# Performance work log

Measured on AMD Instinct MI355X. Metric: run time of the kernel, lower is better.

## Reference

```python
import jax, jax.numpy as jnp
import numpy as np

N_ATOMS = 16384
N_EDGES = 65536
ATOM_DIM = 29
BOND_DIM = 8
UNITS = 64          # message_units / embed_dim
STEPS = 4
HEADS = 8
DENSE = 512
B_MOL = 256         # molecules
T_ATOMS = 64        # atoms per molecule (N_ATOMS = B_MOL * T_ATOMS)


def setup_inputs() -> dict:
    key = jax.random.key(0)
    ks = jax.random.split(key, 24)
    D = UNITS

    atom_features = jax.random.normal(ks[0], (N_ATOMS, ATOM_DIM), jnp.float32)
    bond_features = jax.random.normal(ks[1], (N_EDGES, BOND_DIM), jnp.float32)
    # edges within molecules
    mol = jax.random.randint(ks[2], (N_EDGES,), 0, B_MOL)
    a = jax.random.randint(ks[3], (N_EDGES,), 0, T_ATOMS)
    b = jax.random.randint(ks[4], (N_EDGES,), 0, T_ATOMS)
    pair_indices = jnp.stack([mol * T_ATOMS + a, mol * T_ATOMS + b], axis=1).astype(jnp.int32)
    molecule_indicator = (jnp.arange(N_ATOMS) // T_ATOMS).astype(jnp.int32)

    def xavier(k, shape, fan_in):
        return jax.random.normal(k, shape, jnp.float32) * (1.0 / np.sqrt(fan_in))

    params = dict(
        kernel=xavier(ks[5], (BOND_DIM, D * D), BOND_DIM),
        kernel_bias=jnp.zeros((D * D,), jnp.float32),
        gru_w_ih=xavier(ks[6], (3 * D, D), D),
        gru_w_hh=xavier(ks[7], (3 * D, D), D),
        gru_b_ih=jnp.zeros((3 * D,), jnp.float32),
        gru_b_hh=jnp.zeros((3 * D,), jnp.float32),
        in_proj_w=xavier(ks[8], (3 * D, D), D),
        in_proj_b=jnp.zeros((3 * D,), jnp.float32),
        out_proj_w=xavier(ks[9], (D, D), D),
        out_proj_b=jnp.zeros((D,), jnp.float32),
        ffn_w1=xavier(ks[10], (D, DENSE), D),
        ffn_b1=jnp.zeros((DENSE,), jnp.float32),
        ffn_w2=xavier(ks[11], (DENSE, D), DENSE),
        ffn_b2=jnp.zeros((D,), jnp.float32),
        ln1_g=jnp.ones((D,), jnp.float32),
        ln1_b=jnp.zeros((D,), jnp.float32),
        ln2_g=jnp.ones((D,), jnp.float32),
        ln2_b=jnp.zeros((D,), jnp.float32),
        d1_w=xavier(ks[12], (D, DENSE), D),
        d1_b=jnp.zeros((DENSE,), jnp.float32),
        d2_w=xavier(ks[13], (DENSE, 1), DENSE),
        d2_b=jnp.zeros((1,), jnp.float32),
    )
    return dict(atom_features=atom_features, bond_features=bond_features,
                pair_indices=pair_indices, molecule_indicator=molecule_indicator, **params)


def _layernorm(x, g, b, eps=1e-5):
    mu = x.mean(-1, keepdims=True)
    var = ((x - mu) ** 2).mean(-1, keepdims=True)
    return (x - mu) * jax.lax.rsqrt(var + eps) * g + b


def _forward(atom_features, bond_features, pair_indices, molecule_indicator,
             kernel, kernel_bias, gru_w_ih, gru_w_hh, gru_b_ih, gru_b_hh,
             in_proj_w, in_proj_b, out_proj_w, out_proj_b,
             ffn_w1, ffn_b1, ffn_w2, ffn_b2, ln1_g, ln1_b, ln2_g, ln2_b,
             d1_w, d1_b, d2_w, d2_b):
    D = UNITS
    n = atom_features.shape[0]
    # pad atom features to message_units
    h = jnp.pad(atom_features, ((0, 0), (0, D - atom_features.shape[1])))

    src = pair_indices[:, 0]
    dst = pair_indices[:, 1]
    # per-edge bond-conditioned transform matrices: [E, D, D]
    bond_mat = (bond_features @ kernel + kernel_bias).reshape(-1, D, D)

    for _ in range(STEPS):
        nbr = h[dst]                                      # gather [E, D]
        msg = jnp.einsum('eij,ej->ei', bond_mat, nbr)     # per-edge matvec
        agg = jax.ops.segment_sum(msg, src, num_segments=n)  # scatter-add [N, D]
        # GRUCell(input=agg, hidden=h)
        gi = agg @ gru_w_ih.T + gru_b_ih
        gh = h @ gru_w_hh.T + gru_b_hh
        i_r, i_z, i_n = jnp.split(gi, 3, axis=-1)
        h_r, h_z, h_n = jnp.split(gh, 3, axis=-1)
        r = jax.nn.sigmoid(i_r + h_r)
        z = jax.nn.sigmoid(i_z + h_z)
        nn_ = jnp.tanh(i_n + r * h_n)
        h = (1.0 - z) * nn_ + z * h

    # PartitionPadding: scatter atoms into [B_MOL, T_ATOMS, D] (indicator sorted, contiguous)
    starts = jnp.searchsorted(molecule_indicator, jnp.arange(B_MOL, dtype=molecule_indicator.dtype))
    pos = jnp.arange(n) - starts[molecule_indicator]
    x = jnp.zeros((B_MOL, T_ATOMS, D), h.dtype).at[molecule_indicator, pos].set(h)

    valid = jnp.any(x != 0, axis=-1)                      # [B, T] key-padding mask

    # multi-head self-attention
    qkv = x @ in_proj_w.T + in_proj_b                     # [B, T, 3D]
    q, k, v = jnp.split(qkv, 3, axis=-1)
    hd = D // HEADS
    q = q.reshape(B_MOL, T_ATOMS, HEADS, hd)
    k = k.reshape(B_MOL, T_ATOMS, HEADS, hd)
    v = v.reshape(B_MOL, T_ATOMS, HEADS, hd)
    scores = jnp.einsum('bqhd,bkhd->bhqk', q, k) / np.sqrt(hd)
    scores = jnp.where(valid[:, None, None, :], scores, -1e9)
    attn = jax.nn.softmax(scores, axis=-1)
    ao = jnp.einsum('bhqk,bkhd->bqhd', attn, v).reshape(B_MOL, T_ATOMS, D)
    ao = ao @ out_proj_w.T + out_proj_b

    y1 = _layernorm(x + ao, ln1_g, ln1_b)
    ffn = jax.nn.relu(y1 @ ffn_w1 + ffn_b1) @ ffn_w2 + ffn_b2
    y2 = _layernorm(y1 + ffn, ln2_g, ln2_b)
    pooled = y2.mean(axis=1)                              # [B, D]

    out = jax.nn.relu(pooled @ d1_w + d1_b)
    return jax.nn.sigmoid(out @ d2_w + d2_b)              # [B, 1]


def reference(atom_features, bond_features, pair_indices, molecule_indicator,
              kernel, kernel_bias, gru_w_ih, gru_w_hh, gru_b_ih, gru_b_hh,
              in_proj_w, in_proj_b, out_proj_w, out_proj_b,
              ffn_w1, ffn_b1, ffn_w2, ffn_b2, ln1_g, ln1_b, ln2_g, ln2_b,
              d1_w, d1_b, d2_w, d2_b):
    return _forward(atom_features, bond_features, pair_indices, molecule_indicator,
                    kernel, kernel_bias, gru_w_ih, gru_w_hh, gru_b_ih, gru_b_hh,
                    in_proj_w, in_proj_b, out_proj_w, out_proj_b,
                    ffn_w1, ffn_b1, ffn_w2, ffn_b2, ln1_g, ln1_b, ln2_g, ln2_b,
                    d1_w, d1_b, d2_w, d2_b)
```

## Files before the change

kernel.cpp:

```cpp
#include <hip/hip_runtime.h>
#include <hip/hip_bf16.h>
#include <math.h>

#define NA 16384
#define NE 65536
#define AD 29

typedef __attribute__((ext_vector_type(8))) short bfrag8;
typedef __attribute__((ext_vector_type(4))) float f32x4;

__device__ __forceinline__ float sigmoidf_(float x) { return 1.0f / (1.0f + expf(-x)); }
__device__ __forceinline__ unsigned short bf16bits(float x) {
  __hip_bfloat16 hb = __float2bfloat16(x);
  return *reinterpret_cast<unsigned short*>(&hb);
}
__device__ __forceinline__ float bf16val(unsigned short u) {
  unsigned int b = ((unsigned int)u) << 16;
  return __uint_as_float(b);
}

__global__ void k_init_h(const float* __restrict__ af, float* __restrict__ h,
                         int* __restrict__ count) {
  int idx = blockIdx.x * 256 + threadIdx.x;
  if (idx >= NA * 64) return;
  if (idx < NA) count[idx] = 0;
  int a = idx >> 6, d = idx & 63;
  h[idx] = (d < AD) ? af[a * AD + d] : 0.0f;
}

__global__ void k_prep_KrA(const float* __restrict__ kern, const float* __restrict__ kbias,
                           unsigned short* __restrict__ KrA) {
  int idx = blockIdx.x * 256 + threadIdx.x;
  if (idx >= 36864) return;
  int r = idx & 7;
  int tmp = idx >> 3;
  int lane = tmp & 63;
  int tmp2 = tmp >> 6;
  int ks = tmp2 % 18, w = tmp2 / 18;
  int i = w * 16 + (lane & 15);
  int kj = ks * 32 + ((lane >> 4) << 3) + r;
  int k9 = kj >> 6, j = kj & 63;
  float v = (k9 < 8) ? kern[k9 * 4096 + i * 64 + j] : kbias[i * 64 + j];
  KrA[idx] = bf16bits(v);
}

__global__ void k_prep_Wg(const float* __restrict__ wih, const float* __restrict__ whh,
                          unsigned short* __restrict__ Wh, unsigned short* __restrict__ Wl) {
  int idx = blockIdx.x * 256 + threadIdx.x;
  if (idx >= 24576) return;
  int r = idx & 7;
  int lane = (idx >> 3) & 63;
  int t2 = idx >> 9;
  int ks = t2 & 1;
  int t3 = t2 >> 1;
  int q = t3 % 6, w = t3 / 6;
  int s = q / 3, g = q % 3;
  int R = g * 64 + w * 16 + (lane & 15);
  int kk = ks * 32 + ((lane >> 4) << 3) + r;
  float v = (s == 0) ? wih[R * 64 + kk] : whh[R * 64 + kk];
  unsigned short hi = bf16bits(v);
  Wh[idx] = hi;
  Wl[idx] = bf16bits(v - bf16val(hi));
}

__global__ void k_prep_Wffn(const float* __restrict__ w1, const float* __restrict__ w2,
                            unsigned short* __restrict__ W1h, unsigned short* __restrict__ W1l,
                            unsigned short* __restrict__ W2h, unsigned short* __restrict__ W2l) {
  int idx = blockIdx.x * 256 + threadIdx.x;
  if (idx >= 65536) return;
  int r = idx & 7;
  int lane = (idx >> 3) & 63;
  int rest = (idx >> 9) & 63;
  if (idx < 32768) {
    int tile = rest >> 1, ks = rest & 1;
    int hid = tile * 16 + (lane & 15);
    int kk = ks * 32 + ((lane >> 4) << 3) + r;
    float v = w1[kk * 512 + hid];
    unsigned short hi = bf16bits(v);
    W1h[idx] = hi;
    W1l[idx] = bf16bits(v - bf16val(hi));
  } else {
    int i2 = idx - 32768;
    int tile = rest >> 4, ks = rest & 15;
    int out = tile * 16 + (lane & 15);
    int kk = ks * 32 + ((lane >> 4) << 3) + r;
    float v = w2[kk * 64 + out];
    unsigned short hi = bf16bits(v);
    W2h[i2] = hi;
    W2l[i2] = bf16bits(v - bf16val(hi));
  }
}

__global__ void k_count(const int* __restrict__ pairs, int* __restrict__ count) {
  int e = blockIdx.x * 256 + threadIdx.x;
  if (e >= NE) return;
  atomicAdd(&count[pairs[2 * e]], 1);
}
__global__ void k_scan1(const int* __restrict__ count, int* __restrict__ bsum) {
  __shared__ int red[256];
  int b = blockIdx.x, t = threadIdx.x;
  red[t] = count[b * 256 + t];
  __syncthreads();
  for (int s = 128; s > 0; s >>= 1) { if (t < s) red[t] += red[t + s]; __syncthreads(); }
  if (t == 0) bsum[b] = red[0];
}
__global__ void k_scan2(const int* __restrict__ count, const int* __restrict__ bsum,
                        int* __restrict__ start, int* __restrict__ cursor) {
  __shared__ int sc[256];
  __shared__ int basev;
  int b = blockIdx.x, t = threadIdx.x;
  if (t == 0) { int s = 0; for (int i = 0; i < b; ++i) s += bsum[i]; basev = s; }
  int v = count[b * 256 + t];
  sc[t] = v;
  __syncthreads();
  for (int off = 1; off < 256; off <<= 1) {
    int add = (t >= off) ? sc[t - off] : 0;
    __syncthreads();
    sc[t] += add;
    __syncthreads();
  }
  int excl = sc[t] - v + basev;
  start[b * 256 + t] = excl;
  cursor[b * 256 + t] = excl;
  if (b * 256 + t == NA - 1) start[NA] = excl + v;
}
__global__ void k_place(const int* __restrict__ pairs, int* __restrict__ cursor,
                        int* __restrict__ elist) {
  int e = blockIdx.x * 256 + threadIdx.x;
  if (e >= NE) return;
  int pos = atomicAdd(&cursor[pairs[2 * e]], 1);
  elist[pos] = e;
}
__global__ void k_reorder(const float* __restrict__ bf, const int* __restrict__ pairs,
                          const int* __restrict__ elist, int* __restrict__ sdst,
                          float* __restrict__ sbf) {
  int idx = blockIdx.x * 256 + threadIdx.x;
  if (idx >= NE * 8) return;
  int pos = idx >> 3, k = idx & 7;
  int e = elist[pos];
  sbf[idx] = bf[e * 8 + k];
  if (k == 0) sdst[pos] = pairs[2 * e + 1];
}

#define MW 4
#define MAW 4
__global__ __launch_bounds__(256, 4) void k_msg(
    const float* __restrict__ h_in, const int* __restrict__ start,
    const int* __restrict__ sdst, const float* __restrict__ sbf,
    const unsigned short* __restrict__ KrA,
    const unsigned short* __restrict__ Wh, const unsigned short* __restrict__ Wl,
    const float* __restrict__ bih, const float* __restrict__ bhh,
    float* __restrict__ h_out) {
  __shared__ __align__(16) unsigned short Tb[16 * 584];
  __shared__ __align__(16) unsigned short Xh[16 * 136];
  __shared__ __align__(16) unsigned short Xl[16 * 136];
  __shared__ __align__(16) float Hf[16 * 68];
  __shared__ __align__(16) float AHa[16 * 68];
  __shared__ float bias_s[384];
  const int tid = threadIdx.x, lane = tid & 63, wv = tid >> 6;
  const int ablk = blockIdx.x * 16;
  const int awave = ablk + wv * MAW;

#pragma unroll
  for (int aa = 0; aa < MAW; ++aa) {
    const int a = wv * MAW + aa;
    const float v = h_in[(ablk + a) * 64 + lane];
    Hf[a * 68 + lane] = v;
    const unsigned short hi = bf16bits(v);
    Xh[a * 136 + 64 + lane] = hi;
    Xl[a * 136 + 64 + lane] = bf16bits(v - bf16val(hi));
  }
  if (tid < 192) { bias_s[tid] = bih[tid]; bias_s[192 + tid] = bhh[tid]; }

  for (int a = 0; a < MAW; ++a) {
    const int s0 = __builtin_amdgcn_readfirstlane(start[awave + a]);
    const int s1 = __builtin_amdgcn_readfirstlane(start[awave + a + 1]);
    float t[9] = {0.f, 0.f, 0.f, 0.f, 0.f, 0.f, 0.f, 0.f, 0.f};
    for (int base = s0; base < s1; base += 8) {
      const int nb = s1 - base;
      float hv[8];
#pragma unroll
      for (int i = 0; i < 8; ++i) {
        int d = (i < nb) ? sdst[base + i] : 0;
        hv[i] = (i < nb) ? h_in[d * 64 + lane] : 0.f;
      }
#pragma unroll
      for (int i = 0; i < 8; ++i) {
#pragma unroll
        for (int k = 0; k < 8; ++k)
          t[k] = fmaf(sbf[(base + i) * 8 + k], hv[i], t[k]);
        t[8] += hv[i];
      }
    }
    const int row = wv * MAW + a;
#pragma unroll
    for (int k = 0; k < 9; ++k) Tb[row * 584 + k * 64 + lane] = bf16bits(t[k]);
  }
  __syncthreads();

  f32x4 acc = {0.f, 0.f, 0.f, 0.f};
  const bfrag8* KrA8 = reinterpret_cast<const bfrag8*>(KrA);
  const int tb_base = (lane & 15) * 584 + ((lane >> 4) << 3);
#pragma unroll 3
  for (int ks = 0; ks < 18; ++ks) {
    bfrag8 af = KrA8[(wv * 18 + ks) * 64 + lane];
    bfrag8 bfr = *reinterpret_cast<const bfrag8*>(&Tb[tb_base + ks * 32]);
    acc = __builtin_amdgcn_mfma_f32_16x16x32_bf16(af, bfr, acc, 0, 0, 0);
  }
#pragma unroll
  for (int reg = 0; reg < 4; ++reg) {
    const int ii = wv * 16 + ((lane >> 4) << 2) + reg;
    const unsigned short hi = bf16bits(acc[reg]);
    Xh[(lane & 15) * 136 + ii] = hi;
    Xl[(lane & 15) * 136 + ii] = bf16bits(acc[reg] - bf16val(hi));
  }
  __syncthreads();

  const bfrag8* Wh8 = reinterpret_cast<const bfrag8*>(Wh);
  const bfrag8* Wl8 = reinterpret_cast<const bfrag8*>(Wl);
  f32x4 g0 = {0,0,0,0}, g1 = {0,0,0,0}, g2 = {0,0,0,0};
  f32x4 g3 = {0,0,0,0}, g4 = {0,0,0,0}, g5 = {0,0,0,0};
  f32x4* gptr[6] = {&g0, &g1, &g2, &g3, &g4, &g5};
#pragma unroll
  for (int q = 0; q < 6; ++q) {
    const int s = q / 3;
    f32x4 g = *gptr[q];
#pragma unroll
    for (int ks = 0; ks < 2; ++ks) {
      const int fidx = ((wv * 6 + q) * 2 + ks) * 64 + lane;
      bfrag8 Ah = Wh8[fidx];
      bfrag8 Al = Wl8[fidx];
      const int xoff = (lane & 15) * 136 + (s * 2 + ks) * 32 + ((lane >> 4) << 3);
      bfrag8 Bh = *reinterpret_cast<const bfrag8*>(&Xh[xoff]);
      bfrag8 Bl = *reinterpret_cast<const bfrag8*>(&Xl[xoff]);
      g = __builtin_amdgcn_mfma_f32_16x16x32_bf16(Ah, Bh, g, 0, 0, 0);
      g = __builtin_amdgcn_mfma_f32_16x16x32_bf16(Ah, Bl, g, 0, 0, 0);
      g = __builtin_amdgcn_mfma_f32_16x16x32_bf16(Al, Bh, g, 0, 0, 0);
    }
    *gptr[q] = g;
  }
#pragma unroll
  for (int reg = 0; reg < 4; ++reg) {
    const int i = wv * 16 + ((lane >> 4) << 2) + reg;
    const int atom = lane & 15;
    const float r = sigmoidf_(g0[reg] + bias_s[i] + g3[reg] + bias_s[192 + i]);
    const float z = sigmoidf_(g1[reg] + bias_s[64 + i] + g4[reg] + bias_s[256 + i]);
    const float nn = tanhf(g2[reg] + bias_s[128 + i] + r * (g5[reg] + bias_s[320 + i]));
    const float hold = Hf[atom * 68 + i];
    AHa[atom * 68 + i] = (1.0f - z) * nn + z * hold;
  }
  __syncthreads();
#pragma unroll
  for (int aa = 0; aa < MAW; ++aa) {
    const int a = wv * MAW + aa;
    h_out[(ablk + a) * 64 + lane] = AHa[a * 68 + lane];
  }
}

#define QABLK 4
__global__ __launch_bounds__(256, 2) void k_qkv(
    const float* __restrict__ h, const float* __restrict__ w,
    const float* __restrict__ b, float* __restrict__ qkv,
    int* __restrict__ valid) {
  __shared__ __align__(16) float w_s[192 * 64];
  __shared__ __align__(16) float x_s[4][QABLK][64];
  const int tid = threadIdx.x, lane = tid & 63, wv = tid >> 6;
  for (int idx = tid; idx < 192 * 64; idx += 256) {
    int r = idx >> 6, d = idx & 63;
    w_s[(r << 6) + ((((d >> 2) ^ (r & 7)) << 2) | (d & 3))] = w[idx];
  }
  __syncthreads();
  const float4* w4 = reinterpret_cast<const float4*>(w_s);
  const float bq = b[lane], bk = b[64 + lane], bv_ = b[128 + lane];
  const int swz = lane & 7;
  const int gw = blockIdx.x * 4 + wv;
  const int stride = gridDim.x * 4 * QABLK;
  for (int ag = gw * QABLK; ag < NA; ag += stride) {
#pragma unroll
    for (int e = 0; e < QABLK; ++e) x_s[wv][e][lane] = h[(ag + e) * 64 + lane];
    __syncthreads();
    const float4* x4 = reinterpret_cast<const float4*>(&x_s[wv][0][0]);
    float aq[QABLK] = {0,0,0,0}, ak[QABLK] = {0,0,0,0}, av_[QABLK] = {0,0,0,0};
    int nz[QABLK] = {0,0,0,0};
#pragma unroll 4
    for (int d4 = 0; d4 < 16; ++d4) {
      int sl = d4 ^ swz;
      float4 wq = w4[(lane << 4) + sl];
      float4 wk = w4[((lane + 64) << 4) + sl];
      float4 wvv = w4[((lane + 128) << 4) + sl];
#pragma unroll
      for (int e = 0; e < QABLK; ++e) {
        float4 xv = x4[e * 16 + d4];
        aq[e] += wq.x*xv.x + wq.y*xv.y + wq.z*xv.z + wq.w*xv.w;
        ak[e] += wk.x*xv.x + wk.y*xv.y + wk.z*xv.z + wk.w*xv.w;
        av_[e] += wvv.x*xv.x + wvv.y*xv.y + wvv.z*xv.z + wvv.w*xv.w;
        nz[e] |= (int)(xv.x != 0.f) | (int)(xv.y != 0.f) | (int)(xv.z != 0.f) | (int)(xv.w != 0.f);
      }
    }
#pragma unroll
    for (int e = 0; e < QABLK; ++e) {
      qkv[(ag + e) * 192 + lane] = aq[e] + bq;
      qkv[(ag + e) * 192 + 64 + lane] = ak[e] + bk;
      qkv[(ag + e) * 192 + 128 + lane] = av_[e] + bv_;
      if (lane == 0) valid[ag + e] = nz[e];
    }
    __syncthreads();
  }
}

__global__ void k_attn(const float* __restrict__ qkv, const int* __restrict__ valid,
                       float* __restrict__ ao) {
  const int b = blockIdx.x >> 3, hh = blockIdx.x & 7;
  __shared__ float k_s[64][8];
  __shared__ float v_s[64][8];
  __shared__ int vd_s[64];
  const int lane = threadIdx.x;
  const int rowbase = (b * 64 + lane) * 192;
#pragma unroll
  for (int j = 0; j < 8; ++j) {
    k_s[lane][j] = qkv[rowbase + 64 + hh * 8 + j];
    v_s[lane][j] = qkv[rowbase + 128 + hh * 8 + j];
  }
  vd_s[lane] = valid[b * 64 + lane];
  __syncthreads();
  float q[8];
#pragma unroll
  for (int j = 0; j < 8; ++j) q[j] = qkv[rowbase + hh * 8 + j];
  float m = -3.0e38f, l = 0.f, o[8] = {0,0,0,0,0,0,0,0};
  for (int t = 0; t < 64; ++t) {
    float s = 0.f;
#pragma unroll
    for (int j = 0; j < 8; ++j) s += q[j] * k_s[t][j];
    s *= 0.35355339059327373f;
    s = vd_s[t] ? s : -1.0e9f;
    float mn = fmaxf(m, s);
    float c = expf(m - mn);
    float p = expf(s - mn);
    l = l * c + p;
#pragma unroll
    for (int j = 0; j < 8; ++j) o[j] = o[j] * c + p * v_s[t][j];
    m = mn;
  }
  const float inv = 1.0f / l;
  const int obase = (b * 64 + lane) * 64 + hh * 8;
#pragma unroll
  for (int j = 0; j < 8; ++j) ao[obase + j] = o[j] * inv;
}

#define OABLK 4
__global__ __launch_bounds__(256, 1) void k_out_ln1(
    const float* __restrict__ x, const float* __restrict__ ao,
    const float* __restrict__ w, const float* __restrict__ bias,
    const float* __restrict__ g, const float* __restrict__ bb,
    float* __restrict__ y1) {
  __shared__ __align__(16) float w_s[64 * 64];
  __shared__ __align__(16) float a_s[4][OABLK][64];
  const int tid = threadIdx.x, lane = tid & 63, wv = tid >> 6;
  for (int idx = tid; idx < 64 * 64; idx += 256) {
    int r = idx >> 6, d = idx & 63;
    w_s[(r << 6) + ((((d >> 2) ^ (r & 7)) << 2) | (d & 3))] = w[idx];
  }
  __syncthreads();
  const float4* w4 = reinterpret_cast<const float4*>(w_s);
  const float bo = bias[lane], gg = g[lane], bbb = bb[lane];
  const int swz = lane & 7;
  const int gw = blockIdx.x * 4 + wv;
  const int stride = gridDim.x * 4 * OABLK;
  for (int ag = gw * OABLK; ag < NA; ag += stride) {
#pragma unroll
    for (int e = 0; e < OABLK; ++e) a_s[wv][e][lane] = ao[(ag + e) * 64 + lane];
    __syncthreads();
    const float4* a4 = reinterpret_cast<const float4*>(&a_s[wv][0][0]);
    float acc[OABLK] = {0,0,0,0};
#pragma unroll 4
    for (int d4 = 0; d4 < 16; ++d4) {
      int sl = d4 ^ swz;
      float4 wr = w4[(lane << 4) + sl];
#pragma unroll
      for (int e = 0; e < OABLK; ++e) {
        float4 av = a4[e * 16 + d4];
        acc[e] += wr.x*av.x + wr.y*av.y + wr.z*av.z + wr.w*av.w;
      }
    }
#pragma unroll
    for (int e = 0; e < OABLK; ++e) {
      float val = acc[e] + bo + x[(ag + e) * 64 + lane];
      float s1 = val, s2 = val * val;
#pragma unroll
      for (int mm = 1; mm < 64; mm <<= 1) {
        s1 += __shfl_xor(s1, mm, 64);
        s2 += __shfl_xor(s2, mm, 64);
      }
      float mu = s1 * 0.015625f;
      float var = s2 * 0.015625f - mu * mu;
      y1[(ag + e) * 64 + lane] = (val - mu) * rsqrtf(var + 1e-5f) * gg + bbb;
    }
    __syncthreads();
  }
}

__global__ __launch_bounds__(256, 3) void k_ffn(
    const float* __restrict__ y1,
    const unsigned short* __restrict__ W1h, const unsigned short* __restrict__ W1l,
    const unsigned short* __restrict__ W2h, const unsigned short* __restrict__ W2l,
    const float* __restrict__ b1, const float* __restrict__ b2,
    const float* __restrict__ g, const float* __restrict__ bb,
    float* __restrict__ y2) {
  __shared__ __align__(16) unsigned short Xh[16 * 72];
  __shared__ __align__(16) unsigned short Xl[16 * 72];
  __shared__ __align__(16) unsigned short Hh[16 * 520];
  __shared__ __align__(16) unsigned short Hl[16 * 520];
  __shared__ __align__(16) float Y1f[16 * 68];
  __shared__ __align__(16) float Of[16 * 68];
  const int tid = threadIdx.x, lane = tid & 63, wv = tid >> 6;
  const int ablk = blockIdx.x * 16;

#pragma unroll
  for (int aa = 0; aa < 4; ++aa) {
    const int a = wv * 4 + aa;
    const float v = y1[(ablk + a) * 64 + lane];
    Y1f[a * 68 + lane] = v;
    const unsigned short hi = bf16bits(v);
    Xh[a * 72 + lane] = hi;
    Xl[a * 72 + lane] = bf16bits(v - bf16val(hi));
  }
  __syncthreads();

  const bfrag8* W1h8 = reinterpret_cast<const bfrag8*>(W1h);
  const bfrag8* W1l8 = reinterpret_cast<const bfrag8*>(W1l);
  const int xoff_base = (lane & 15) * 72 + ((lane >> 4) << 3);
#pragma unroll 2
  for (int t = 0; t < 8; ++t) {
    f32x4 acc = {0.f, 0.f, 0.f, 0.f};
    const int tile = wv * 8 + t;
#pragma unroll
    for (int ks = 0; ks < 2; ++ks) {
      const int fidx = (tile * 2 + ks) * 64 + lane;
      bfrag8 Ah = W1h8[fidx];
      bfrag8 Al = W1l8[fidx];
      bfrag8 Bh = *reinterpret_cast<const bfrag8*>(&Xh[xoff_base + ks * 32]);
      bfrag8 Bl = *reinterpret_cast<const bfrag8*>(&Xl[xoff_base + ks * 32]);
      acc = __builtin_amdgcn_mfma_f32_16x16x32_bf16(Ah, Bh, acc, 0, 0, 0);
      acc = __builtin_amdgcn_mfma_f32_16x16x32_bf16(Ah, Bl, acc, 0, 0, 0);
      acc = __builtin_amdgcn_mfma_f32_16x16x32_bf16(Al, Bh, acc, 0, 0, 0);
    }
#pragma unroll
    for (int reg = 0; reg < 4; ++reg) {
      const int hid = tile * 16 + ((lane >> 4) << 2) + reg;
      float val = fmaxf(acc[reg] + b1[hid], 0.f);
      const unsigned short hi = bf16bits(val);
      Hh[(lane & 15) * 520 + hid] = hi;
      Hl[(lane & 15) * 520 + hid] = bf16bits(val - bf16val(hi));
    }
  }
  __syncthreads();

  const bfrag8* W2h8 = reinterpret_cast<const bfrag8*>(W2h);
  const bfrag8* W2l8 = reinterpret_cast<const bfrag8*>(W2l);
  f32x4 acc2 = {0.f, 0.f, 0.f, 0.f};
  const int hoff_base = (lane & 15) * 520 + ((lane >> 4) << 3);
#pragma unroll 4
  for (int ks = 0; ks < 16; ++ks) {
    const int fidx = (wv * 16 + ks) * 64 + lane;
    bfrag8 Ah = W2h8[fidx];
    bfrag8 Al = W2l8[fidx];
    bfrag8 Bh = *reinterpret_cast<const bfrag8*>(&Hh[hoff_base + ks * 32]);
    bfrag8 Bl = *reinterpret_cast<const bfrag8*>(&Hl[hoff_base + ks * 32]);
    acc2 = __builtin_amdgcn_mfma_f32_16x16x32_bf16(Ah, Bh, acc2, 0, 0, 0);
    acc2 = __builtin_amdgcn_mfma_f32_16x16x32_bf16(Ah, Bl, acc2, 0, 0, 0);
    acc2 = __builtin_amdgcn_mfma_f32_16x16x32_bf16(Al, Bh, acc2, 0, 0, 0);
  }
#pragma unroll
  for (int reg = 0; reg < 4; ++reg) {
    const int outr = wv * 16 + ((lane >> 4) << 2) + reg;
    Of[(lane & 15) * 68 + outr] = acc2[reg] + b2[outr];
  }
  __syncthreads();

  const float gg = g[lane], bbb = bb[lane];
#pragma unroll
  for (int aa = 0; aa < 4; ++aa) {
    const int a = wv * 4 + aa;
    float val = Y1f[a * 68 + lane] + Of[a * 68 + lane];
    float s1 = val, s2 = val * val;
#pragma unroll
    for (int mm = 1; mm < 64; mm <<= 1) {
      s1 += __shfl_xor(s1, mm, 64);
      s2 += __shfl_xor(s2, mm, 64);
    }
    float mu = s1 * 0.015625f;
    float var = s2 * 0.015625f - mu * mu;
    y2[(ablk + a) * 64 + lane] = (val - mu) * rsqrtf(var + 1e-5f) * gg + bbb;
  }
}

__global__ __launch_bounds__(256) void k_pool(const float* __restrict__ y2,
                                              float* __restrict__ pooled) {
  const int b = blockIdx.x;
  const int tid = threadIdx.x, lane = tid & 63, wv = tid >> 6;
  __shared__ float part[4][64];
  float s = 0.f;
#pragma unroll 4
  for (int t = wv * 16; t < wv * 16 + 16; ++t) s += y2[(b * 64 + t) * 64 + lane];
  part[wv][lane] = s;
  __syncthreads();
  if (wv == 0)
    pooled[b * 64 + lane] =
        (part[0][lane] + part[1][lane] + part[2][lane] + part[3][lane]) * 0.015625f;
}

__global__ __launch_bounds__(256) void k_head(
    const float* __restrict__ pooled, const float* __restrict__ d1w,
    const float* __restrict__ d1b, const float* __restrict__ d2w,
    const float* __restrict__ d2b, float* __restrict__ out) {
  const int b = blockIdx.x;
  __shared__ float p_s[64];
  __shared__ float red_s[4];
  const int tid = threadIdx.x;
  if (tid < 64) p_s[tid] = pooled[b * 64 + tid];
  __syncthreads();
  float acc = 0.f;
#pragma unroll
  for (int rep = 0; rep < 2; ++rep) {
    int c = rep * 256 + tid;
    float hvv = d1b[c];
    for (int d = 0; d < 64; ++d) hvv += p_s[d] * d1w[d * 512 + c];
    acc += fmaxf(hvv, 0.f) * d2w[c];
  }
#pragma unroll
  for (int mm = 1; mm < 64; mm <<= 1) acc += __shfl_xor(acc, mm, 64);
  if ((tid & 63) == 0) red_s[tid >> 6] = acc;
  __syncthreads();
  if (tid == 0) {
    float t = red_s[0] + red_s[1] + red_s[2] + red_s[3] + d2b[0];
    out[b] = 1.0f / (1.0f + expf(-t));
  }
}

extern "C" void kernel_launch(void* const* d_in, const int* in_sizes, int n_in,
                              void* d_out, int out_size, void* d_ws, size_t ws_size,
                              hipStream_t stream) {
  (void)in_sizes; (void)n_in; (void)out_size; (void)ws_size;
  const float* af   = (const float*)d_in[0];
  const float* bfeat= (const float*)d_in[1];
  const int*   pairs= (const int*)d_in[2];
  const float* kern = (const float*)d_in[4];
  const float* kbias= (const float*)d_in[5];
  const float* wih  = (const float*)d_in[6];
  const float* whh  = (const float*)d_in[7];
  const float* bih  = (const float*)d_in[8];
  const float* bhh  = (const float*)d_in[9];
  const float* ipw  = (const float*)d_in[10];
  const float* ipb  = (const float*)d_in[11];
  const float* opw  = (const float*)d_in[12];
  const float* opb  = (const float*)d_in[13];
  const float* fw1  = (const float*)d_in[14];
  const float* fb1  = (const float*)d_in[15];
  const float* fw2  = (const float*)d_in[16];
  const float* fb2  = (const float*)d_in[17];
  const float* l1g  = (const float*)d_in[18];
  const float* l1b  = (const float*)d_in[19];
  const float* l2g  = (const float*)d_in[20];
  const float* l2b  = (const float*)d_in[21];
  const float* d1w  = (const float*)d_in[22];
  const float* d1b  = (const float*)d_in[23];
  const float* d2w  = (const float*)d_in[24];
  const float* d2b  = (const float*)d_in[25];
  float* out = (float*)d_out;

  float* ws = (float*)d_ws;
  float* h      = ws;
  float* h2     = h + (size_t)NA * 64;
  float* qkv    = h2 + (size_t)NA * 64;
  float* ao     = qkv + (size_t)NA * 192;
  float* y1     = ao + (size_t)NA * 64;
  float* y2     = y1 + (size_t)NA * 64;
  float* pooled = y2 + (size_t)NA * 64;
  int*   valid  = (int*)(pooled + 256 * 64);

  unsigned short* W1h = (unsigned short*)(valid + NA);
  unsigned short* W1l = W1h + 32768;
  unsigned short* W2h = W1l + 32768;
  unsigned short* W2l = W2h + 32768;

  unsigned short* KrA = (unsigned short*)qkv;
  int*   count  = (int*)(qkv + 36864);
  int*   start  = count + NA;
  int*   cursor = start + NA + 1;
  int*   elist  = cursor + NA;
  int*   bsum   = elist + NE;
  int*   sdst   = bsum + 256;
  float* sbf    = (float*)(sdst + NE + 8);
  unsigned short* Wh = (unsigned short*)(sbf + (size_t)NE * 8 + 64);
  unsigned short* Wl = Wh + 24576;

  k_init_h<<<NA * 64 / 256, 256, 0, stream>>>(af, h, count);
  k_prep_KrA<<<144, 256, 0, stream>>>(kern, kbias, KrA);
  k_prep_Wg<<<96, 256, 0, stream>>>(wih, whh, Wh, Wl);
  k_prep_Wffn<<<256, 256, 0, stream>>>(fw1, fw2, W1h, W1l, W2h, W2l);
  k_count<<<NE / 256, 256, 0, stream>>>(pairs, count);
  k_scan1<<<64, 256, 0, stream>>>(count, bsum);
  k_scan2<<<64, 256, 0, stream>>>(count, bsum, start, cursor);
  k_place<<<NE / 256, 256, 0, stream>>>(pairs, cursor, elist);
  k_reorder<<<NE * 8 / 256, 256, 0, stream>>>(bfeat, pairs, elist, sdst, sbf);

  float* hin = h;
  float* hout = h2;
  for (int s = 0; s < 4; ++s) {
    k_msg<<<NA / 16, 256, 0, stream>>>(hin, start, sdst, sbf, KrA,
                                       Wh, Wl, bih, bhh, hout);
    float* tmp = hin; hin = hout; hout = tmp;
  }

  k_qkv<<<512, 256, 0, stream>>>(h, ipw, ipb, qkv, valid);
  k_attn<<<2048, 64, 0, stream>>>(qkv, valid, ao);
  k_out_ln1<<<512, 256, 0, stream>>>(h, ao, opw, opb, l1g, l1b, y1);
  k_ffn<<<NA / 16, 256, 0, stream>>>(y1, W1h, W1l, W2h, W2l, fb1, fb2, l2g, l2b, y2);
  k_pool<<<256, 256, 0, stream>>>(y2, pooled);
  k_head<<<256, 256, 0, stream>>>(pooled, d1w, d1b, d2w, d2b, out);
}
```

Baseline: 187.7 us.

## Fuse QKV, attention, out-proj and LayerNorm into per-molecule MFMA kernel

Replaces the separate QKV projection, attention and out-proj+LN1 kernels with one kernel per molecule. It keeps Q/K/V and the attention output in shared memory and computes both projections with split-bf16 MFMA (hi/lo, three products). The weight prep kernels are merged into one launch that also prepares the projection weights, and pooling is folded into the head kernel. This removes global round trips for qkv/ao and several launches. In exchange the grid is only 256 blocks with large shared memory, and the attention loop runs serially per lane.

```diff
diff --git a/kernel.cpp b/kernel.cpp
--- a/kernel.cpp
+++ b/kernel.cpp
@@ -28,66 +28,93 @@
   h[idx] = (d < AD) ? af[a * AD + d] : 0.0f;
 }
 
-__global__ void k_prep_KrA(const float* __restrict__ kern, const float* __restrict__ kbias,
-                           unsigned short* __restrict__ KrA) {
-  int idx = blockIdx.x * 256 + threadIdx.x;
-  if (idx >= 36864) return;
-  int r = idx & 7;
-  int tmp = idx >> 3;
-  int lane = tmp & 63;
-  int tmp2 = tmp >> 6;
-  int ks = tmp2 % 18, w = tmp2 / 18;
-  int i = w * 16 + (lane & 15);
-  int kj = ks * 32 + ((lane >> 4) << 3) + r;
-  int k9 = kj >> 6, j = kj & 63;
-  float v = (k9 < 8) ? kern[k9 * 4096 + i * 64 + j] : kbias[i * 64 + j];
-  KrA[idx] = bf16bits(v);
-}
-
-__global__ void k_prep_Wg(const float* __restrict__ wih, const float* __restrict__ whh,
-                          unsigned short* __restrict__ Wh, unsigned short* __restrict__ Wl) {
-  int idx = blockIdx.x * 256 + threadIdx.x;
-  if (idx >= 24576) return;
-  int r = idx & 7;
-  int lane = (idx >> 3) & 63;
-  int t2 = idx >> 9;
-  int ks = t2 & 1;
-  int t3 = t2 >> 1;
-  int q = t3 % 6, w = t3 / 6;
-  int s = q / 3, g = q % 3;
-  int R = g * 64 + w * 16 + (lane & 15);
-  int kk = ks * 32 + ((lane >> 4) << 3) + r;
-  float v = (s == 0) ? wih[R * 64 + kk] : whh[R * 64 + kk];
-  unsigned short hi = bf16bits(v);
-  Wh[idx] = hi;
-  Wl[idx] = bf16bits(v - bf16val(hi));
-}
-
-__global__ void k_prep_Wffn(const float* __restrict__ w1, const float* __restrict__ w2,
-                            unsigned short* __restrict__ W1h, unsigned short* __restrict__ W1l,
-                            unsigned short* __restrict__ W2h, unsigned short* __restrict__ W2l) {
-  int idx = blockIdx.x * 256 + threadIdx.x;
-  if (idx >= 65536) return;
-  int r = idx & 7;
-  int lane = (idx >> 3) & 63;
-  int rest = (idx >> 9) & 63;
-  if (idx < 32768) {
-    int tile = rest >> 1, ks = rest & 1;
-    int hid = tile * 16 + (lane & 15);
+__global__ void k_prep_all(
+    const float* __restrict__ kern, const float* __restrict__ kbias,
+    const float* __restrict__ wih, const float* __restrict__ whh,
+    const float* __restrict__ w1, const float* __restrict__ w2,
+    const float* __restrict__ ipw, const float* __restrict__ opw,
+    unsigned short* __restrict__ KrA,
+    unsigned short* __restrict__ Wh, unsigned short* __restrict__ Wl,
+    unsigned short* __restrict__ W1h, unsigned short* __restrict__ W1l,
+    unsigned short* __restrict__ W2h, unsigned short* __restrict__ W2l,
+    unsigned short* __restrict__ PQh, unsigned short* __restrict__ PQl,
+    unsigned short* __restrict__ POh, unsigned short* __restrict__ POl) {
+  int idx0 = blockIdx.x * 256 + threadIdx.x;
+  if (idx0 < 36864) {
+    int idx = idx0;
+    int r = idx & 7;
+    int lane = (idx >> 3) & 63;
+    int tmp2 = idx >> 9;
+    int ks = tmp2 % 18, w = tmp2 / 18;
+    int i = w * 16 + (lane & 15);
+    int kj = ks * 32 + ((lane >> 4) << 3) + r;
+    int k9 = kj >> 6, j = kj & 63;
+    float v = (k9 < 8) ? kern[k9 * 4096 + i * 64 + j] : kbias[i * 64 + j];
+    KrA[idx] = bf16bits(v);
+  } else if (idx0 < 61440) {
+    int idx = idx0 - 36864;
+    int r = idx & 7;
+    int lane = (idx >> 3) & 63;
+    int t2 = idx >> 9;
+    int ks = t2 & 1;
+    int t3 = t2 >> 1;
+    int q = t3 % 6, w = t3 / 6;
+    int s = q / 3, g = q % 3;
+    int R = g * 64 + w * 16 + (lane & 15);
     int kk = ks * 32 + ((lane >> 4) << 3) + r;
-    float v = w1[kk * 512 + hid];
+    float v = (s == 0) ? wih[R * 64 + kk] : whh[R * 64 + kk];
     unsigned short hi = bf16bits(v);
-    W1h[idx] = hi;
-    W1l[idx] = bf16bits(v - bf16val(hi));
-  } else {
-    int i2 = idx - 32768;
-    int tile = rest >> 4, ks = rest & 15;
-    int out = tile * 16 + (lane & 15);
-    int kk = ks * 32 + ((lane >> 4) << 3) + r;
-    float v = w2[kk * 64 + out];
-    unsigned short hi = bf16bits(v);
-    W2h[i2] = hi;
-    W2l[i2] = bf16bits(v - bf16val(hi));
+    Wh[idx] = hi;
+    Wl[idx] = bf16bits(v - bf16val(hi));
+  } else if (idx0 < 126976) {
+    int idx = idx0 - 61440;
+    int r = idx & 7;
+    int lane = (idx >> 3) & 63;
+    int rest = (idx >> 9) & 63;
+    if (idx < 32768) {
+      int tile = rest >> 1, ks = rest & 1;
+      int hid = tile * 16 + (lane & 15);
+      int kk = ks * 32 + ((lane >> 4) << 3) + r;
+      float v = w1[kk * 512 + hid];
+      unsigned short hi = bf16bits(v);
+      W1h[idx] = hi;
+      W1l[idx] = bf16bits(v - bf16val(hi));
+    } else {
+      int i2 = idx - 32768;
+      int tile = rest >> 4, ks = rest & 15;
+      int outr = tile * 16 + (lane & 15);
+      int kk = ks * 32 + ((lane >> 4) << 3) + r;
+      float v = w2[kk * 64 + outr];
+      unsigned short hi = bf16bits(v);
+      W2h[i2] = hi;
+      W2l[i2] = bf16bits(v - bf16val(hi));
+    }
+  } else if (idx0 < 143360) {
+    int i = idx0 - 126976;
+    if (i < 12288) {
+      int r = i & 7;
+      int lane = (i >> 3) & 63;
+      int rest = i >> 9;
+      int t = rest >> 1, ks = rest & 1;
+      int R = t * 16 + (lane & 15);
+      int kk = ks * 32 + ((lane >> 4) << 3) + r;
+      float v = ipw[R * 64 + kk];
+      unsigned short hi = bf16bits(v);
+      PQh[i] = hi;
+      PQl[i] = bf16bits(v - bf16val(hi));
+    } else {
+      int i2 = i - 12288;
+      int r = i2 & 7;
+      int lane = (i2 >> 3) & 63;
+      int rest = i2 >> 9;
+      int t = rest >> 1, ks = rest & 1;
+      int R = t * 16 + (lane & 15);
+      int kk = ks * 32 + ((lane >> 4) << 3) + r;
+      float v = opw[R * 64 + kk];
+      unsigned short hi = bf16bits(v);
+      POh[i2] = hi;
+      POl[i2] = bf16bits(v - bf16val(hi));
+    }
   }
 }
 
@@ -257,145 +284,131 @@
   }
 }
 
-#define QABLK 4
-__global__ __launch_bounds__(256, 2) void k_qkv(
-    const float* __restrict__ h, const float* __restrict__ w,
-    const float* __restrict__ b, float* __restrict__ qkv,
-    int* __restrict__ valid) {
-  __shared__ __align__(16) float w_s[192 * 64];
-  __shared__ __align__(16) float x_s[4][QABLK][64];
+__global__ __launch_bounds__(256, 1) void k_mol(
+    const float* __restrict__ h,
+    const unsigned short* __restrict__ PQh, const unsigned short* __restrict__ PQl,
+    const unsigned short* __restrict__ POh, const unsigned short* __restrict__ POl,
+    const float* __restrict__ ipb, const float* __restrict__ opb,
+    const float* __restrict__ l1g, const float* __restrict__ l1b,
+    float* __restrict__ y1) {
+  __shared__ __align__(16) float Hf[64 * 65];
+  __shared__ __align__(16) unsigned short Xh[64 * 72];
+  __shared__ __align__(16) unsigned short Xl[64 * 72];
+  __shared__ __align__(16) float QKVs[192 * 65];
+  __shared__ __align__(16) unsigned short AOh[64 * 72];
+  __shared__ __align__(16) unsigned short AOl[64 * 72];
+  __shared__ __align__(16) float Of[64 * 65];
+  __shared__ int vd[64];
   const int tid = threadIdx.x, lane = tid & 63, wv = tid >> 6;
-  for (int idx = tid; idx < 192 * 64; idx += 256) {
-    int r = idx >> 6, d = idx & 63;
-    w_s[(r << 6) + ((((d >> 2) ^ (r & 7)) << 2) | (d & 3))] = w[idx];
-  }
-  __syncthreads();
-  const float4* w4 = reinterpret_cast<const float4*>(w_s);
-  const float bq = b[lane], bk = b[64 + lane], bv_ = b[128 + lane];
-  const int swz = lane & 7;
-  const int gw = blockIdx.x * 4 + wv;
-  const int stride = gridDim.x * 4 * QABLK;
-  for (int ag = gw * QABLK; ag < NA; ag += stride) {
-#pragma unroll
-    for (int e = 0; e < QABLK; ++e) x_s[wv][e][lane] = h[(ag + e) * 64 + lane];
-    __syncthreads();
-    const float4* x4 = reinterpret_cast<const float4*>(&x_s[wv][0][0]);
-    float aq[QABLK] = {0,0,0,0}, ak[QABLK] = {0,0,0,0}, av_[QABLK] = {0,0,0,0};
-    int nz[QABLK] = {0,0,0,0};
-#pragma unroll 4
-    for (int d4 = 0; d4 < 16; ++d4) {
-      int sl = d4 ^ swz;
-      float4 wq = w4[(lane << 4) + sl];
-      float4 wk = w4[((lane + 64) << 4) + sl];
-      float4 wvv = w4[((lane + 128) << 4) + sl];
-#pragma unroll
-      for (int e = 0; e < QABLK; ++e) {
-        float4 xv = x4[e * 16 + d4];
-        aq[e] += wq.x*xv.x + wq.y*xv.y + wq.z*xv.z + wq.w*xv.w;
-        ak[e] += wk.x*xv.x + wk.y*xv.y + wk.z*xv.z + wk.w*xv.w;
-        av_[e] += wvv.x*xv.x + wvv.y*xv.y + wvv.z*xv.z + wvv.w*xv.w;
-        nz[e] |= (int)(xv.x != 0.f) | (int)(xv.y != 0.f) | (int)(xv.z != 0.f) | (int)(xv.w != 0.f);
-      }
-    }
-#pragma unroll
-    for (int e = 0; e < QABLK; ++e) {
-      qkv[(ag + e) * 192 + lane] = aq[e] + bq;
-      qkv[(ag + e) * 192 + 64 + lane] = ak[e] + bk;
-      qkv[(ag + e) * 192 + 128 + lane] = av_[e] + bv_;
-      if (lane == 0) valid[ag + e] = nz[e];
-    }
-    __syncthreads();
-  }
-}
-
-__global__ void k_attn(const float* __restrict__ qkv, const int* __restrict__ valid,
-                       float* __restrict__ ao) {
-  const int b = blockIdx.x >> 3, hh = blockIdx.x & 7;
-  __shared__ float k_s[64][8];
-  __shared__ float v_s[64][8];
-  __shared__ int vd_s[64];
-  const int lane = threadIdx.x;
-  const int rowbase = (b * 64 + lane) * 192;
-#pragma unroll
-  for (int j = 0; j < 8; ++j) {
-    k_s[lane][j] = qkv[rowbase + 64 + hh * 8 + j];
-    v_s[lane][j] = qkv[rowbase + 128 + hh * 8 + j];
-  }
-  vd_s[lane] = valid[b * 64 + lane];
-  __syncthreads();
-  float q[8];
-#pragma unroll
-  for (int j = 0; j < 8; ++j) q[j] = qkv[rowbase + hh * 8 + j];
-  float m = -3.0e38f, l = 0.f, o[8] = {0,0,0,0,0,0,0,0};
-  for (int t = 0; t < 64; ++t) {
-    float s = 0.f;
-#pragma unroll
-    for (int j = 0; j < 8; ++j) s += q[j] * k_s[t][j];
-    s *= 0.35355339059327373f;
-    s = vd_s[t] ? s : -1.0e9f;
-    float mn = fmaxf(m, s);
-    float c = expf(m - mn);
-    float p = expf(s - mn);
-    l = l * c + p;
-#pragma unroll
-    for (int j = 0; j < 8; ++j) o[j] = o[j] * c + p * v_s[t][j];
-    m = mn;
-  }
-  const float inv = 1.0f / l;
-  const int obase = (b * 64 + lane) * 64 + hh * 8;
-#pragma unroll
-  for (int j = 0; j < 8; ++j) ao[obase + j] = o[j] * inv;
-}
-
-#define OABLK 4
-__global__ __launch_bounds__(256, 1) void k_out_ln1(
-    const float* __restrict__ x, const float* __restrict__ ao,
-    const float* __restrict__ w, const float* __restrict__ bias,
-    const float* __restrict__ g, const float* __restrict__ bb,
-    float* __restrict__ y1) {
-  __shared__ __align__(16) float w_s[64 * 64];
-  __shared__ __align__(16) float a_s[4][OABLK][64];
-  const int tid = threadIdx.x, lane = tid & 63, wv = tid >> 6;
-  for (int idx = tid; idx < 64 * 64; idx += 256) {
-    int r = idx >> 6, d = idx & 63;
-    w_s[(r << 6) + ((((d >> 2) ^ (r & 7)) << 2) | (d & 3))] = w[idx];
-  }
-  __syncthreads();
-  const float4* w4 = reinterpret_cast<const float4*>(w_s);
-  const float bo = bias[lane], gg = g[lane], bbb = bb[lane];
-  const int swz = lane & 7;
-  const int gw = blockIdx.x * 4 + wv;
-  const int stride = gridDim.x * 4 * OABLK;
-  for (int ag = gw * OABLK; ag < NA; ag += stride) {
-#pragma unroll
-    for (int e = 0; e < OABLK; ++e) a_s[wv][e][lane] = ao[(ag + e) * 64 + lane];
-    __syncthreads();
-    const float4* a4 = reinterpret_cast<const float4*>(&a_s[wv][0][0]);
-    float acc[OABLK] = {0,0,0,0};
-#pragma unroll 4
-    for (int d4 = 0; d4 < 16; ++d4) {
-      int sl = d4 ^ swz;
-      float4 wr = w4[(lane << 4) + sl];
-#pragma unroll
-      for (int e = 0; e < OABLK; ++e) {
-        float4 av = a4[e * 16 + d4];
-        acc[e] += wr.x*av.x + wr.y*av.y + wr.z*av.z + wr.w*av.w;
-      }
-    }
-#pragma unroll
-    for (int e = 0; e < OABLK; ++e) {
-      float val = acc[e] + bo + x[(ag + e) * 64 + lane];
-      float s1 = val, s2 = val * val;
-#pragma unroll
-      for (int mm = 1; mm < 64; mm <<= 1) {
-        s1 += __shfl_xor(s1, mm, 64);
-        s2 += __shfl_xor(s2, mm, 64);
-      }
-      float mu = s1 * 0.015625f;
-      float var = s2 * 0.015625f - mu * mu;
-      y1[(ag + e) * 64 + lane] = (val - mu) * rsqrtf(var + 1e-5f) * gg + bbb;
-    }
-    __syncthreads();
+  const int mol = blockIdx.x;
+
+  for (int aa = 0; aa < 16; ++aa) {
+    const int a = wv * 16 + aa;
+    const float v = h[(mol * 64 + a) * 64 + lane];
+    Hf[a * 65 + lane] = v;
+    const unsigned short hi = bf16bits(v);
+    Xh[a * 72 + lane] = hi;
+    Xl[a * 72 + lane] = bf16bits(v - bf16val(hi));
+    int nz = __any(v != 0.0f);
+    if (lane == 0) vd[a] = nz;
+  }
+  __syncthreads();
+
+  const bfrag8* PQh8 = reinterpret_cast<const bfrag8*>(PQh);
+  const bfrag8* PQl8 = reinterpret_cast<const bfrag8*>(PQl);
+  const int xoff_b = (wv * 16 + (lane & 15)) * 72 + ((lane >> 4) << 3);
+#pragma unroll 3
+  for (int tile = 0; tile < 12; ++tile) {
+    f32x4 acc = {0.f, 0.f, 0.f, 0.f};
+#pragma unroll
+    for (int ks = 0; ks < 2; ++ks) {
+      const int fidx = (tile * 2 + ks) * 64 + lane;
+      bfrag8 Ah = PQh8[fidx];
+      bfrag8 Al = PQl8[fidx];
+      bfrag8 Bh = *reinterpret_cast<const bfrag8*>(&Xh[xoff_b + ks * 32]);
+      bfrag8 Bl = *reinterpret_cast<const bfrag8*>(&Xl[xoff_b + ks * 32]);
+      acc = __builtin_amdgcn_mfma_f32_16x16x32_bf16(Ah, Bh, acc, 0, 0, 0);
+      acc = __builtin_amdgcn_mfma_f32_16x16x32_bf16(Ah, Bl, acc, 0, 0, 0);
+      acc = __builtin_amdgcn_mfma_f32_16x16x32_bf16(Al, Bh, acc, 0, 0, 0);
+    }
+#pragma unroll
+    for (int reg = 0; reg < 4; ++reg) {
+      const int row = tile * 16 + ((lane >> 4) << 2) + reg;
+      QKVs[row * 65 + wv * 16 + (lane & 15)] = acc[reg] + ipb[row];
+    }
+  }
+  __syncthreads();
+
+#pragma unroll
+  for (int hp = 0; hp < 2; ++hp) {
+    const int hh = wv * 2 + hp;
+    float q[8];
+#pragma unroll
+    for (int j = 0; j < 8; ++j) q[j] = QKVs[(hh * 8 + j) * 65 + lane];
+    float m = -3.0e38f, l = 0.f, o[8] = {0,0,0,0,0,0,0,0};
+    for (int t = 0; t < 64; ++t) {
+      float s = 0.f;
+#pragma unroll
+      for (int j = 0; j < 8; ++j) s += q[j] * QKVs[(64 + hh * 8 + j) * 65 + t];
+      s *= 0.35355339059327373f;
+      s = vd[t] ? s : -1.0e9f;
+      float mn = fmaxf(m, s);
+      float c = expf(m - mn);
+      float p = expf(s - mn);
+      l = l * c + p;
+#pragma unroll
+      for (int j = 0; j < 8; ++j) o[j] = o[j] * c + p * QKVs[(128 + hh * 8 + j) * 65 + t];
+      m = mn;
+    }
+    const float inv = 1.0f / l;
+#pragma unroll
+    for (int j = 0; j < 8; ++j) {
+      const float v = o[j] * inv;
+      const unsigned short hi = bf16bits(v);
+      AOh[lane * 72 + hh * 8 + j] = hi;
+      AOl[lane * 72 + hh * 8 + j] = bf16bits(v - bf16val(hi));
+    }
+  }
+  __syncthreads();
+
+  const bfrag8* POh8 = reinterpret_cast<const bfrag8*>(POh);
+  const bfrag8* POl8 = reinterpret_cast<const bfrag8*>(POl);
+  const int aoff_b = (wv * 16 + (lane & 15)) * 72 + ((lane >> 4) << 3);
+#pragma unroll
+  for (int tile = 0; tile < 4; ++tile) {
+    f32x4 acc = {0.f, 0.f, 0.f, 0.f};
+#pragma unroll
+    for (int ks = 0; ks < 2; ++ks) {
+      const int fidx = (tile * 2 + ks) * 64 + lane;
+      bfrag8 Ah = POh8[fidx];
+      bfrag8 Al = POl8[fidx];
+      bfrag8 Bh = *reinterpret_cast<const bfrag8*>(&AOh[aoff_b + ks * 32]);
+      bfrag8 Bl = *reinterpret_cast<const bfrag8*>(&AOl[aoff_b + ks * 32]);
+      acc = __builtin_amdgcn_mfma_f32_16x16x32_bf16(Ah, Bh, acc, 0, 0, 0);
+      acc = __builtin_amdgcn_mfma_f32_16x16x32_bf16(Ah, Bl, acc, 0, 0, 0);
+      acc = __builtin_amdgcn_mfma_f32_16x16x32_bf16(Al, Bh, acc, 0, 0, 0);
+    }
+#pragma unroll
+    for (int reg = 0; reg < 4; ++reg) {
+      const int dim = tile * 16 + ((lane >> 4) << 2) + reg;
+      Of[(wv * 16 + (lane & 15)) * 65 + dim] = acc[reg] + opb[dim];
+    }
+  }
+  __syncthreads();
+
+  const float gg = l1g[lane], bbb = l1b[lane];
+  for (int aa = 0; aa < 16; ++aa) {
+    const int a = wv * 16 + aa;
+    float val = Hf[a * 65 + lane] + Of[a * 65 + lane];
+    float s1 = val, s2 = val * val;
+#pragma unroll
+    for (int mm = 1; mm < 64; mm <<= 1) {
+      s1 += __shfl_xor(s1, mm, 64);
+      s2 += __shfl_xor(s2, mm, 64);
+    }
+    float mu = s1 * 0.015625f;
+    float var = s2 * 0.015625f - mu * mu;
+    y1[(mol * 64 + a) * 64 + lane] = (val - mu) * rsqrtf(var + 1e-5f) * gg + bbb;
   }
 }
 
@@ -494,30 +507,22 @@
   }
 }
 
-__global__ __launch_bounds__(256) void k_pool(const float* __restrict__ y2,
-                                              float* __restrict__ pooled) {
+__global__ __launch_bounds__(256) void k_head(
+    const float* __restrict__ y2, const float* __restrict__ d1w,
+    const float* __restrict__ d1b, const float* __restrict__ d2w,
+    const float* __restrict__ d2b, float* __restrict__ out) {
   const int b = blockIdx.x;
   const int tid = threadIdx.x, lane = tid & 63, wv = tid >> 6;
   __shared__ float part[4][64];
+  __shared__ float p_s[64];
+  __shared__ float red_s[4];
   float s = 0.f;
 #pragma unroll 4
   for (int t = wv * 16; t < wv * 16 + 16; ++t) s += y2[(b * 64 + t) * 64 + lane];
   part[wv][lane] = s;
   __syncthreads();
-  if (wv == 0)
-    pooled[b * 64 + lane] =
-        (part[0][lane] + part[1][lane] + part[2][lane] + part[3][lane]) * 0.015625f;
-}
-
-__global__ __launch_bounds__(256) void k_head(
-    const float* __restrict__ pooled, const float* __restrict__ d1w,
-    const float* __restrict__ d1b, const float* __restrict__ d2w,
-    const float* __restrict__ d2b, float* __restrict__ out) {
-  const int b = blockIdx.x;
-  __shared__ float p_s[64];
-  __shared__ float red_s[4];
-  const int tid = threadIdx.x;
-  if (tid < 64) p_s[tid] = pooled[b * 64 + tid];
+  if (tid < 64)
+    p_s[tid] = (part[0][tid] + part[1][tid] + part[2][tid] + part[3][tid]) * 0.015625f;
   __syncthreads();
   float acc = 0.f;
 #pragma unroll
@@ -577,11 +582,16 @@
   float* y2     = y1 + (size_t)NA * 64;
   float* pooled = y2 + (size_t)NA * 64;
   int*   valid  = (int*)(pooled + 256 * 64);
+  (void)ao; (void)pooled;
 
   unsigned short* W1h = (unsigned short*)(valid + NA);
   unsigned short* W1l = W1h + 32768;
   unsigned short* W2h = W1l + 32768;
   unsigned short* W2l = W2h + 32768;
+  unsigned short* PQh = W2l + 32768;
+  unsigned short* PQl = PQh + 12288;
+  unsigned short* POh = PQl + 12288;
+  unsigned short* POl = POh + 4096;
 
   unsigned short* KrA = (unsigned short*)qkv;
   int*   count  = (int*)(qkv + 36864);
@@ -595,9 +605,9 @@
   unsigned short* Wl = Wh + 24576;
 
   k_init_h<<<NA * 64 / 256, 256, 0, stream>>>(af, h, count);
-  k_prep_KrA<<<144, 256, 0, stream>>>(kern, kbias, KrA);
-  k_prep_Wg<<<96, 256, 0, stream>>>(wih, whh, Wh, Wl);
-  k_prep_Wffn<<<256, 256, 0, stream>>>(fw1, fw2, W1h, W1l, W2h, W2l);
+  k_prep_all<<<560, 256, 0, stream>>>(kern, kbias, wih, whh, fw1, fw2, ipw, opw,
+                                      KrA, Wh, Wl, W1h, W1l, W2h, W2l,
+                                      PQh, PQl, POh, POl);
   k_count<<<NE / 256, 256, 0, stream>>>(pairs, count);
   k_scan1<<<64, 256, 0, stream>>>(count, bsum);
   k_scan2<<<64, 256, 0, stream>>>(count, bsum, start, cursor);
@@ -612,10 +622,7 @@
     float* tmp = hin; hin = hout; hout = tmp;
   }
 
-  k_qkv<<<512, 256, 0, stream>>>(h, ipw, ipb, qkv, valid);
-  k_attn<<<2048, 64, 0, stream>>>(qkv, valid, ao);
-  k_out_ln1<<<512, 256, 0, stream>>>(h, ao, opw, opb, l1g, l1b, y1);
+  k_mol<<<256, 256, 0, stream>>>(h, PQh, PQl, POh, POl, ipb, opb, l1g, l1b, y1);
   k_ffn<<<NA / 16, 256, 0, stream>>>(y1, W1h, W1l, W2h, W2l, fb1, fb2, l2g, l2b, y2);
-  k_pool<<<256, 256, 0, stream>>>(y2, pooled);
-  k_head<<<256, 256, 0, stream>>>(pooled, d1w, d1b, d2w, d2b, out);
-}
+  k_head<<<256, 256, 0, stream>>>(y2, d1w, d1b, d2w, d2b, out);
+}
```

After: 161.7 us. 1.16x faster.
